# Performance work log

Measured on AMD Instinct MI355X. Metric: run time of the kernel, lower is better.

Reference implementation:

```python
import jax, jax.numpy as jnp
import numpy as np

B, N, K, D, H, PQ, PV = 2, 2048, 30, 128, 4, 8, 4
INV3C = float(np.sqrt(1.0 / (3 * D)))      # 1/sqrt(3*hidden_dim)
INV3 = float(np.sqrt(1.0 / 3.0))
PT_SCALE = float(np.sqrt(1.0 / (3 * (PQ * 9.0 / 2))))


def _gather(nodes, idx):
    # nodes [B,N,...], idx [B,N,K] -> [B,N,K,...]
    return jax.vmap(lambda n, i: n[i])(nodes, idx)


def _ln(x, w, b, eps=1e-5):
    mu = x.mean(-1, keepdims=True)
    var = x.var(-1, keepdims=True)
    return (x - mu) / jnp.sqrt(var + eps) * w + b


def _forward(h_V, h_E, E_idx, R, t, mask_attend, mask_V,
             Wq, bq, Wkv, bkv, Wqp, bqp, Wkvp, bkvp, Wb, bb_, head_weights,
             Wout, bout, ln0_w, ln0_b, ln1_w, ln1_b, Wm1, bm1, Wm2, bm2):
    q = (h_V @ Wq + bq).reshape(B, N, H, D)                     # [B,N,H,C]
    kv = (h_V @ Wkv + bkv).reshape(B, N, H, 2 * D)
    k_, v_ = kv[..., :D], kv[..., D:]

    def apply_rigid(pts):  # pts [B,N,P,3] -> R @ p + t
        return jnp.einsum('bnxy,bnpy->bnpx', R, pts) + t[:, :, None, :]

    # torch builds points by split-into-3-then-stack along last dim
    qp = h_V @ Wqp + bqp                                        # [B,N,H*PQ*3]
    q_pts = jnp.stack(jnp.split(qp, 3, axis=-1), axis=-1)       # [B,N,H*PQ,3]
    q_pts = apply_rigid(q_pts).reshape(B, N, H, PQ, 3)
    kvp = h_V @ Wkvp + bkvp
    kv_pts = jnp.stack(jnp.split(kvp, 3, axis=-1), axis=-1)
    kv_pts = apply_rigid(kv_pts).reshape(B, N, H, PQ + PV, 3)
    k_pts, v_pts = kv_pts[..., :PQ, :], kv_pts[..., PQ:, :]

    b_bias = h_E @ Wb + bb_                                     # [B,N,K,H]
    k_nb = _gather(k_, E_idx)                                   # [B,N,K,H,C]
    a = jnp.einsum('bnhc,bnkhc->bnkh', q, k_nb) * INV3C
    a = a + INV3 * b_bias

    kp_nb = _gather(k_pts, E_idx)                               # [B,N,K,H,PQ,3]
    diff = q_pts[:, :, None] - kp_nb
    pt_att = jnp.sum(diff * diff, axis=-1)                      # [B,N,K,H,PQ]
    hw = jax.nn.softplus(head_weights)                          # [H]
    pt_att = jnp.sum(PT_SCALE * hw[None, None, None, :, None] * pt_att, axis=-1) * -0.5

    att_mask = 100000.0 * (mask_attend - 1.0)                   # [B,N,K]
    a = a + pt_att + att_mask[..., None]
    a = jax.nn.softmax(a, axis=-2)                              # softmax over neighbors K

    v_nb = _gather(v_, E_idx)
    o = jnp.einsum('bnkh,bnkhc->bnhc', a, v_nb).reshape(B, N, H * D)
    vp_nb = _gather(v_pts, E_idx)                               # [B,N,K,H,PV,3]
    o_pt = jnp.einsum('bnkh,bnkhpx->bnhpx', a, vp_nb)
    # invert_apply: R^T (x - t)
    o_pt = jnp.einsum('bnyx,bnhpy->bnhpx', R, o_pt - t[:, :, None, None, :])
    o_pt_norm = jnp.sqrt(jnp.sum(o_pt ** 2, axis=-1) + 1e-8).reshape(B, N, H * PV)
    o_pt = o_pt.reshape(B, N, H * PV, 3)
    o_pair = jnp.einsum('bnkh,bnkc->bnhc', a, h_E).reshape(B, N, H * D)

    cat = jnp.concatenate([o, o_pt[..., 0], o_pt[..., 1], o_pt[..., 2], o_pt_norm, o_pair], axis=-1)
    s = cat @ Wout + bout

    hv = _ln(h_V + s, ln0_w, ln0_b)
    m = jax.nn.relu(hv @ Wm1 + bm1) @ Wm2 + bm2
    hv = _ln(hv + m, ln1_w, ln1_b)
    return hv * mask_V[..., None]


def setup_inputs() -> dict:
    key = jax.random.key(0)
    ks = jax.random.split(key, 16)

    def dense(k, fi, fo):
        kw, kb = jax.random.split(k)
        s = 1.0 / np.sqrt(fi)
        return (jax.random.uniform(kw, (fi, fo), jnp.float32, -s, s),
                jax.random.uniform(kb, (fo,), jnp.float32, -s, s))

    h_V = jax.random.normal(ks[0], (B, N, D), jnp.float32)
    h_E = jax.random.normal(ks[1], (B, N, K, D), jnp.float32)
    E_idx = jax.random.randint(ks[2], (B, N, K), 0, N)
    Rr = jax.random.normal(ks[3], (B, N, 3, 3), jnp.float32)
    R, _ = jnp.linalg.qr(Rr)  # proper orthonormal frames
    t = jax.random.normal(ks[4], (B, N, 3), jnp.float32)
    mask_attend = jnp.ones((B, N, K), jnp.float32)
    mask_V = jnp.ones((B, N), jnp.float32)

    Wq, bq = dense(ks[5], D, D * H)
    Wkv, bkv = dense(ks[6], D, 2 * D * H)
    Wqp, bqp = dense(ks[7], D, H * PQ * 3)
    Wkvp, bkvp = dense(ks[8], D, H * (PQ + PV) * 3)
    Wb, bb_ = dense(ks[9], D, H)
    head_weights = jnp.full((H,), 0.541324854612918, jnp.float32)
    out_dim = H * (D + D + 4 * PV)
    Wout, bout = dense(ks[10], out_dim, D)
    ln0_w = jnp.ones((D,), jnp.float32); ln0_b = jnp.zeros((D,), jnp.float32)
    ln1_w = jnp.ones((D,), jnp.float32); ln1_b = jnp.zeros((D,), jnp.float32)
    Wm1, bm1 = dense(ks[11], D, 4 * D)
    Wm2, bm2 = dense(ks[12], 4 * D, D)
    return dict(h_V=h_V, h_E=h_E, E_idx=E_idx, R=R, t=t,
                mask_attend=mask_attend, mask_V=mask_V,
                Wq=Wq, bq=bq, Wkv=Wkv, bkv=bkv, Wqp=Wqp, bqp=bqp,
                Wkvp=Wkvp, bkvp=bkvp, Wb=Wb, bb_=bb_, head_weights=head_weights,
                Wout=Wout, bout=bout, ln0_w=ln0_w, ln0_b=ln0_b,
                ln1_w=ln1_w, ln1_b=ln1_b, Wm1=Wm1, bm1=bm1, Wm2=Wm2, bm2=bm2)


def reference(h_V, h_E, E_idx, R, t, mask_attend, mask_V,
              Wq, bq, Wkv, bkv, Wqp, bqp, Wkvp, bkvp, Wb, bb_, head_weights,
              Wout, bout, ln0_w, ln0_b, ln1_w, ln1_b, Wm1, bm1, Wm2, bm2):
    return _forward(h_V, h_E, E_idx, R, t, mask_attend, mask_V,
                    Wq, bq, Wkv, bkv, Wqp, bqp, Wkvp, bkvp, Wb, bb_, head_weights,
                    Wout, bout, ln0_w, ln0_b, ln1_w, ln1_b, Wm1, bm1, Wm2, bm2)
```

## Files before the change

kernel.cpp:

```cpp
#include <hip/hip_runtime.h>
#include <math.h>

#define BB 2
#define NN 2048
#define KK 30
#define DD 128
#define HH 4
#define PQ_ 8
#define PV_ 4
#define TM 16

#define INV3C    0.05103103630798288f
#define INV3     0.5773502691896258f
#define PT_SCALE 0.09622504486493764f

typedef __attribute__((ext_vector_type(8))) short short8;
typedef __attribute__((ext_vector_type(4))) float f32x4;
typedef unsigned short ushort_t;

__device__ __forceinline__ ushort_t f2bf(float f) {
    unsigned u = __float_as_uint(f);
    unsigned r = u + 0x7FFFu + ((u >> 16) & 1u);
    return (ushort_t)(r >> 16);
}
__device__ __forceinline__ float bf2f(ushort_t u) {
    return __uint_as_float(((unsigned)u) << 16);
}
__device__ __forceinline__ float bflo(unsigned u) {
    return __uint_as_float(u << 16);
}
__device__ __forceinline__ float bfhi(unsigned u) {
    return __uint_as_float(u & 0xffff0000u);
}

__global__ __launch_bounds__(256) void prep_kernel(
    const float* __restrict__ Wout, const float* __restrict__ Wm1,
    const float* __restrict__ Wm2,
    const float* __restrict__ Wq, const float* __restrict__ Wkv,
    const float* __restrict__ Wqp, const float* __restrict__ Wkvp,
    ushort_t* __restrict__ WoutT, ushort_t* __restrict__ Wm1T,
    ushort_t* __restrict__ Wm2T, ushort_t* __restrict__ WprojT)
{
    const int stride = gridDim.x * blockDim.x;
    const int t0 = blockIdx.x * blockDim.x + threadIdx.x;
    for (int idx = t0; idx < 128 * 1088; idx += stride) {
        int n = idx / 1088, k = idx - n * 1088;
        WoutT[idx] = f2bf(Wout[(size_t)k * 128 + n]);
    }
    for (int idx = t0; idx < 512 * 128; idx += stride) {
        int n = idx >> 7, k = idx & 127;
        Wm1T[idx] = f2bf(Wm1[(size_t)k * 512 + n]);
    }
    for (int idx = t0; idx < 128 * 512; idx += stride) {
        int n = idx >> 9, k = idx & 511;
        Wm2T[idx] = f2bf(Wm2[(size_t)k * 128 + n]);
    }
    for (int idx = t0; idx < 1792 * 128; idx += stride) {
        int n = idx >> 7, k = idx & 127;
        float v;
        if (n < 512)       v = Wq[(size_t)k * 512 + n];
        else if (n < 1536) v = Wkv[(size_t)k * 1024 + (n - 512)];
        else if (n < 1632) v = Wqp[k * 96 + (n - 1536)];
        else if (n < 1776) v = Wkvp[k * 144 + (n - 1632)];
        else               v = 0.f;
        WprojT[idx] = f2bf(v);
    }
}

__global__ __launch_bounds__(512) void proj_kernel(
    const float* __restrict__ hV, const float* __restrict__ R, const float* __restrict__ tvec,
    const ushort_t* __restrict__ WT,
    const float* __restrict__ bq, const float* __restrict__ bkv,
    const float* __restrict__ bqp, const float* __restrict__ bkvp,
    ushort_t* __restrict__ qb, ushort_t* __restrict__ kb, ushort_t* __restrict__ vb,
    float* __restrict__ qpts, float* __restrict__ kpts, float* __restrict__ vpts)
{
    const int node0 = (blockIdx.x >> 1) * TM;
    const int half  = blockIdx.x & 1;
    const int tid = threadIdx.x;
    const int w = tid >> 6, l = tid & 63, lr = l & 15, lk = l >> 4;

    __shared__ ushort_t s_A[TM][128];
    __shared__ float s_qp[TM][96];
    __shared__ float s_kvp[TM][144];

    {
        int i = tid * 4; int r = i >> 7, c = i & 127;
        float4 x = *(const float4*)&hV[(size_t)(node0 + r) * DD + c];
        s_A[r][c + 0] = f2bf(x.x); s_A[r][c + 1] = f2bf(x.y);
        s_A[r][c + 2] = f2bf(x.z); s_A[r][c + 3] = f2bf(x.w);
    }
    __syncthreads();

    const ushort_t* Ab = &s_A[lr][lk * 8];
    for (int t = 0; t < 7; ++t) {
        const int tile = half * 56 + w * 7 + t;
        const int n = tile * 16 + lr;
        f32x4 acc = {0.f, 0.f, 0.f, 0.f};
        const ushort_t* Bb = WT + (size_t)n * 128 + lk * 8;
        #pragma unroll
        for (int ks = 0; ks < 4; ++ks) {
            short8 a = *(const short8*)(Ab + ks * 32);
            short8 bfr = *(const short8*)(Bb + ks * 32);
            acc = __builtin_amdgcn_mfma_f32_16x16x32_bf16(a, bfr, acc, 0, 0, 0);
        }
        if (n < 512) {
            float bias = bq[n];
            #pragma unroll
            for (int i = 0; i < 4; ++i)
                qb[(size_t)(node0 + lk * 4 + i) * 512 + n] = f2bf(acc[i] + bias);
        } else if (n < 1536) {
            int n2 = n - 512;
            float bias = bkv[n2];
            int hh = n2 >> 8, wcol = n2 & 255;
            ushort_t* base = (wcol < 128) ? kb : vb;
            int off = hh * DD + (wcol & 127);
            #pragma unroll
            for (int i = 0; i < 4; ++i)
                base[(size_t)(node0 + lk * 4 + i) * 512 + off] = f2bf(acc[i] + bias);
        } else if (n < 1632) {
            int c = n - 1536;
            float bias = bqp[c];
            #pragma unroll
            for (int i = 0; i < 4; ++i) s_qp[lk * 4 + i][c] = acc[i] + bias;
        } else if (n < 1776) {
            int c = n - 1632;
            float bias = bkvp[c];
            #pragma unroll
            for (int i = 0; i < 4; ++i) s_kvp[lk * 4 + i][c] = acc[i] + bias;
        }
    }
    __syncthreads();

    if (half == 1) {
        for (int idx = tid; idx < TM * 96; idx += 512) {
            int r = idx / 96, u = idx % 96;
            int j = u / 3, d = u % 3;
            int node = node0 + r;
            float acc = tvec[node * 3 + d];
            #pragma unroll
            for (int y = 0; y < 3; ++y)
                acc = fmaf(R[node * 9 + d * 3 + y], s_qp[r][y * 32 + j], acc);
            qpts[(size_t)node * 96 + j * 3 + d] = acc;
        }
        for (int idx = tid; idx < TM * 144; idx += 512) {
            int r = idx / 144, u = idx % 144;
            int jj = u / 3, d = u % 3;
            int node = node0 + r;
            float acc = tvec[node * 3 + d];
            #pragma unroll
            for (int y = 0; y < 3; ++y)
                acc = fmaf(R[node * 9 + d * 3 + y], s_kvp[r][y * 48 + jj], acc);
            int hh = jj / 12, pp = jj % 12;
            if (pp < PQ_) kpts[(size_t)node * 96 + (hh * PQ_ + pp) * 3 + d] = acc;
            else          vpts[(size_t)node * 48 + (hh * PV_ + (pp - PQ_)) * 3 + d] = acc;
        }
    }
}

__global__ __launch_bounds__(256, 6) void attn_kernel(
    const float* __restrict__ hE, const int* __restrict__ Eidx,
    const float* __restrict__ R, const float* __restrict__ tvec,
    const float* __restrict__ mask_att,
    const float* __restrict__ Wb, const float* __restrict__ bb,
    const float* __restrict__ head_w,
    const ushort_t* __restrict__ qb, const ushort_t* __restrict__ kb,
    const ushort_t* __restrict__ vb,
    const float* __restrict__ qpts, const float* __restrict__ kpts, const float* __restrict__ vpts,
    ushort_t* __restrict__ catb)
{
    const int node = blockIdx.x;
    const int b = node >> 11;
    const int tid = threadIdx.x;
    const int lane = tid & 63;
    const int wv = tid >> 6;

    __shared__ ushort_t s_hEb[KK * DD];
    __shared__ float s_cat[1088];
    __shared__ float s_qp[96];
    __shared__ float s_p[HH][32];
    __shared__ int   s_j[32];
    __shared__ float s_mask[32];
    __shared__ float s_opt[48];

    if (tid < 96) s_qp[tid] = qpts[(size_t)node * 96 + tid];
    if (tid < KK) {
        s_j[tid] = Eidx[(size_t)node * KK + tid];
        s_mask[tid] = 100000.0f * (mask_att[(size_t)node * KK + tid] - 1.0f);
    }
    __syncthreads();

    const int h = wv;
    const int l32 = lane & 31;
    const int g = lane >> 5;
    const float* hE_node = hE + (size_t)node * (KK * DD);

    const unsigned qu0 = *(const unsigned*)&qb[(size_t)node * 512 + h * DD + 2 * l32];
    const unsigned qu1 = *(const unsigned*)&qb[(size_t)node * 512 + h * DD + 64 + 2 * l32];
    const float q0 = bflo(qu0), q1 = bfhi(qu0), q2 = bflo(qu1), q3 = bfhi(qu1);
    const float wb0 = Wb[(l32 +  0) * HH + h];
    const float wb1 = Wb[(l32 + 32) * HH + h];
    const float wb2 = Wb[(l32 + 64) * HH + h];
    const float wb3 = Wb[(l32 + 96) * HH + h];
    const float cpt = -0.5f * PT_SCALE * log1pf(expf(head_w[h]));
    const float bbh = INV3 * bb[h];
    const float qpl = (l32 < 24) ? s_qp[h * 24 + l32] : 0.f;

    #pragma unroll
    for (int kx2 = 0; kx2 < KK / 2; ++kx2) {
        const int k = kx2 * 2 + g;
        size_t jb = (size_t)(b * NN + s_j[k]);
        const ushort_t* kr = kb + jb * 512 + h * DD;
        unsigned ku0 = *(const unsigned*)&kr[2 * l32];
        unsigned ku1 = *(const unsigned*)&kr[64 + 2 * l32];
        float s = q0 * bflo(ku0) + q1 * bfhi(ku0) + q2 * bflo(ku1) + q3 * bfhi(ku1);
        const float* her = hE_node + k * DD;
        float h0 = her[l32], h1 = her[l32 + 32], h2 = her[l32 + 64], h3 = her[l32 + 96];
        if (wv == 0) {
            s_hEb[k * DD + l32]      = f2bf(h0);
            s_hEb[k * DD + l32 + 32] = f2bf(h1);
            s_hEb[k * DD + l32 + 64] = f2bf(h2);
            s_hEb[k * DD + l32 + 96] = f2bf(h3);
        }
        float t = wb0 * h0 + wb1 * h1 + wb2 * h2 + wb3 * h3;
        float ptc = 0.f;
        if (l32 < 24) {
            float d = qpl - kpts[jb * 96 + h * 24 + l32];
            ptc = d * d;
        }
        float val = INV3C * s + INV3 * t + cpt * ptc;
        #pragma unroll
        for (int off = 16; off; off >>= 1) val += __shfl_down(val, off, 32);
        if (l32 == 0) s_p[h][k] = val + bbh + s_mask[k];
    }
    __syncthreads();

    {
        float v = (lane < KK) ? s_p[h][lane] : -INFINITY;
        float m = v;
        #pragma unroll
        for (int off = 16; off; off >>= 1) m = fmaxf(m, __shfl_down(m, off));
        m = __shfl(m, 0);
        float e = (lane < KK) ? expf(v - m) : 0.f;
        float s = e;
        #pragma unroll
        for (int off = 16; off; off >>= 1) s += __shfl_down(s, off);
        s = __shfl(s, 0);
        if (lane < KK) s_p[h][lane] = e / s;
    }
    __syncthreads();

    {
        const int oh = tid >> 6;
        const int oc0 = (tid & 63) * 2;
        const ushort_t* vrow = vb + oh * DD + oc0;
        float a0 = 0.f, a1 = 0.f, b0 = 0.f, b1 = 0.f;
        #pragma unroll
        for (int kx = 0; kx < KK; ++kx) {
            unsigned pv = *(const unsigned*)(vrow + (size_t)(b * NN + s_j[kx]) * 512);
            unsigned pe = *(const unsigned*)&s_hEb[kx * DD + oc0];
            float p = s_p[oh][kx];
            a0 = fmaf(p, bflo(pv), a0);
            a1 = fmaf(p, bfhi(pv), a1);
            b0 = fmaf(p, bflo(pe), b0);
            b1 = fmaf(p, bfhi(pe), b1);
        }
        s_cat[oh * DD + oc0]           = a0;
        s_cat[oh * DD + oc0 + 1]       = a1;
        s_cat[576 + oh * DD + oc0]     = b0;
        s_cat[576 + oh * DD + oc0 + 1] = b1;
    }
    if (tid < 48) {
        const int oh = (tid / 3) >> 2;
        float acc = 0.f;
        #pragma unroll
        for (int kx = 0; kx < KK; ++kx)
            acc = fmaf(s_p[oh][kx], vpts[(size_t)(b * NN + s_j[kx]) * 48 + tid], acc);
        s_opt[tid] = acc;
    }
    __syncthreads();
    if (tid < 16) {
        int jj = tid;
        float g0 = s_opt[jj * 3 + 0] - tvec[node * 3 + 0];
        float g1 = s_opt[jj * 3 + 1] - tvec[node * 3 + 1];
        float g2 = s_opt[jj * 3 + 2] - tvec[node * 3 + 2];
        float l0 = R[node * 9 + 0] * g0 + R[node * 9 + 3] * g1 + R[node * 9 + 6] * g2;
        float l1 = R[node * 9 + 1] * g0 + R[node * 9 + 4] * g1 + R[node * 9 + 7] * g2;
        float l2 = R[node * 9 + 2] * g0 + R[node * 9 + 5] * g1 + R[node * 9 + 8] * g2;
        s_cat[512 + 0 * 16 + jj] = l0;
        s_cat[512 + 1 * 16 + jj] = l1;
        s_cat[512 + 2 * 16 + jj] = l2;
        s_cat[560 + jj] = sqrtf(l0 * l0 + l1 * l1 + l2 * l2 + 1e-8f);
    }
    __syncthreads();

    for (int i = tid; i < 1088; i += 256)
        catb[(size_t)node * 1088 + i] = f2bf(s_cat[i]);
}

__global__ __launch_bounds__(512) void tail_kernel(
    const float* __restrict__ hV, const float* __restrict__ maskV,
    const ushort_t* __restrict__ catb,
    const ushort_t* __restrict__ WoutT, const float* __restrict__ bout,
    const float* __restrict__ ln0w, const float* __restrict__ ln0b,
    const float* __restrict__ ln1w, const float* __restrict__ ln1b,
    const ushort_t* __restrict__ Wm1T, const float* __restrict__ bm1,
    const ushort_t* __restrict__ Wm2T, const float* __restrict__ bm2,
    float* __restrict__ out)
{
    const int node0 = blockIdx.x * TM;
    const int tid = threadIdx.x;
    const int w  = tid >> 6;
    const int l  = tid & 63;
    const int lr = l & 15;
    const int lk = l >> 4;

    __shared__ float    s_x[TM][DD];
    __shared__ float    s_hv[TM][DD];
    __shared__ ushort_t s_hvb[TM][136];
    __shared__ ushort_t s_m1[TM][520];
    __shared__ float    s_rs[TM][16];
    __shared__ float    s_rq[TM][16];
    __shared__ float    s_stat[TM][2];

    {
        f32x4 acc = {0.f, 0.f, 0.f, 0.f};
        const ushort_t* Ab = catb + (size_t)(node0 + lr) * 1088 + lk * 8;
        const ushort_t* Bb = WoutT + (size_t)(w * 16 + lr) * 1088 + lk * 8;
        #pragma unroll 2
        for (int ks = 0; ks < 34; ++ks) {
            short8 a = *(const short8*)(Ab + ks * 32);
            short8 bfr = *(const short8*)(Bb + ks * 32);
            acc = __builtin_amdgcn_mfma_f32_16x16x32_bf16(a, bfr, acc, 0, 0, 0);
        }
        #pragma unroll
        for (int i = 0; i < 4; ++i)
            s_x[lk * 4 + i][w * 16 + lr] = acc[i];
    }
    __syncthreads();

    if (tid < 256) {
        int r = tid >> 4, sg = tid & 15;
        float ss = 0.f, sq = 0.f;
        #pragma unroll
        for (int j = 0; j < 8; ++j) {
            int cc = sg * 8 + j;
            float x = s_x[r][cc] + bout[cc] + hV[(size_t)(node0 + r) * DD + cc];
            s_x[r][cc] = x;
            ss += x; sq += x * x;
        }
        s_rs[r][sg] = ss; s_rq[r][sg] = sq;
    }
    __syncthreads();
    if (tid < TM) {
        float ss = 0.f, sq = 0.f;
        #pragma unroll
        for (int sg = 0; sg < 16; ++sg) { ss += s_rs[tid][sg]; sq += s_rq[tid][sg]; }
        float mu = ss / 128.f;
        s_stat[tid][0] = mu;
        s_stat[tid][1] = rsqrtf(sq / 128.f - mu * mu + 1e-5f);
    }
    __syncthreads();
    {
        int idx = tid * 4;
        int r = idx >> 7, cc = idx & 127;
        float mu = s_stat[r][0], rstd = s_stat[r][1];
        #pragma unroll
        for (int j = 0; j < 4; ++j) {
            float hvv = (s_x[r][cc + j] - mu) * rstd * ln0w[cc + j] + ln0b[cc + j];
            s_hv[r][cc + j] = hvv;
            s_hvb[r][cc + j] = f2bf(hvv);
        }
    }
    __syncthreads();

    {
        const ushort_t* Ab = &s_hvb[lr][lk * 8];
        #pragma unroll
        for (int t = 0; t < 4; ++t) {
            int n0 = w * 64 + t * 16;
            f32x4 acc = {0.f, 0.f, 0.f, 0.f};
            const ushort_t* Bb = Wm1T + (size_t)(n0 + lr) * 128 + lk * 8;
            #pragma unroll
            for (int ks = 0; ks < 4; ++ks) {
                short8 a = *(const short8*)(Ab + ks * 32);
                short8 bfr = *(const short8*)(Bb + ks * 32);
                acc = __builtin_amdgcn_mfma_f32_16x16x32_bf16(a, bfr, acc, 0, 0, 0);
            }
            int n = n0 + lr;
            float bm = bm1[n];
            #pragma unroll
            for (int i = 0; i < 4; ++i)
                s_m1[lk * 4 + i][n] = f2bf(fmaxf(acc[i] + bm, 0.f));
        }
    }
    __syncthreads();

    {
        f32x4 acc = {0.f, 0.f, 0.f, 0.f};
        const ushort_t* Ab = &s_m1[lr][lk * 8];
        const ushort_t* Bb = Wm2T + (size_t)(w * 16 + lr) * 512 + lk * 8;
        #pragma unroll 4
        for (int ks = 0; ks < 16; ++ks) {
            short8 a = *(const short8*)(Ab + ks * 32);
            short8 bfr = *(const short8*)(Bb + ks * 32);
            acc = __builtin_amdgcn_mfma_f32_16x16x32_bf16(a, bfr, acc, 0, 0, 0);
        }
        #pragma unroll
        for (int i = 0; i < 4; ++i)
            s_x[lk * 4 + i][w * 16 + lr] = acc[i];
    }
    __syncthreads();

    if (tid < 256) {
        int r = tid >> 4, sg = tid & 15;
        float ss = 0.f, sq = 0.f;
        #pragma unroll
        for (int j = 0; j < 8; ++j) {
            int cc = sg * 8 + j;
            float x = s_x[r][cc] + bm2[cc] + s_hv[r][cc];
            s_x[r][cc] = x;
            ss += x; sq += x * x;
        }
        s_rs[r][sg] = ss; s_rq[r][sg] = sq;
    }
    __syncthreads();
    if (tid < TM) {
        float ss = 0.f, sq = 0.f;
        #pragma unroll
        for (int sg = 0; sg < 16; ++sg) { ss += s_rs[tid][sg]; sq += s_rq[tid][sg]; }
        float mu = ss / 128.f;
        s_stat[tid][0] = mu;
        s_stat[tid][1] = rsqrtf(sq / 128.f - mu * mu + 1e-5f);
    }
    __syncthreads();
    {
        int idx = tid * 4;
        int r = idx >> 7, cc = idx & 127;
        float mu = s_stat[r][0], rstd = s_stat[r][1];
        float mk = maskV[node0 + r];
        float4 o;
        o.x = ((s_x[r][cc + 0] - mu) * rstd * ln1w[cc + 0] + ln1b[cc + 0]) * mk;
        o.y = ((s_x[r][cc + 1] - mu) * rstd * ln1w[cc + 1] + ln1b[cc + 1]) * mk;
        o.z = ((s_x[r][cc + 2] - mu) * rstd * ln1w[cc + 2] + ln1b[cc + 2]) * mk;
        o.w = ((s_x[r][cc + 3] - mu) * rstd * ln1w[cc + 3] + ln1b[cc + 3]) * mk;
        *(float4*)&out[(size_t)(node0 + r) * DD + cc] = o;
    }
}

extern "C" void kernel_launch(void* const* d_in, const int* in_sizes, int n_in,
                              void* d_out, int out_size, void* d_ws, size_t ws_size,
                              hipStream_t stream)
{
    const float* hV      = (const float*)d_in[0];
    const float* hE      = (const float*)d_in[1];
    const int*   Eidx    = (const int*)  d_in[2];
    const float* R       = (const float*)d_in[3];
    const float* tvec    = (const float*)d_in[4];
    const float* mask_at = (const float*)d_in[5];
    const float* maskV   = (const float*)d_in[6];
    const float* Wq      = (const float*)d_in[7];
    const float* bq      = (const float*)d_in[8];
    const float* Wkv     = (const float*)d_in[9];
    const float* bkv     = (const float*)d_in[10];
    const float* Wqp     = (const float*)d_in[11];
    const float* bqp     = (const float*)d_in[12];
    const float* Wkvp    = (const float*)d_in[13];
    const float* bkvp    = (const float*)d_in[14];
    const float* Wb      = (const float*)d_in[15];
    const float* bb      = (const float*)d_in[16];
    const float* hw      = (const float*)d_in[17];
    const float* Wout    = (const float*)d_in[18];
    const float* bout    = (const float*)d_in[19];
    const float* ln0w    = (const float*)d_in[20];
    const float* ln0b    = (const float*)d_in[21];
    const float* ln1w    = (const float*)d_in[22];
    const float* ln1b    = (const float*)d_in[23];
    const float* Wm1     = (const float*)d_in[24];
    const float* bm1     = (const float*)d_in[25];
    const float* Wm2     = (const float*)d_in[26];
    const float* bm2     = (const float*)d_in[27];

    const size_t nodes = (size_t)BB * NN;
    ushort_t* qb     = (ushort_t*)d_ws;
    ushort_t* kb     = qb + nodes * 512;
    ushort_t* vb     = kb + nodes * 512;
    ushort_t* catb   = vb + nodes * 512;
    ushort_t* WoutT  = catb + nodes * 1088;
    ushort_t* Wm1T   = WoutT + 128 * 1088;
    ushort_t* Wm2T   = Wm1T + 512 * 128;
    ushort_t* WprojT = Wm2T + 128 * 512;
    float* qpts = (float*)(WprojT + 1792 * 128);
    float* kpts = qpts + nodes * 96;
    float* vpts = kpts + nodes * 96;

    prep_kernel<<<256, 256, 0, stream>>>(Wout, Wm1, Wm2, Wq, Wkv, Wqp, Wkvp,
                                         WoutT, Wm1T, Wm2T, WprojT);

    proj_kernel<<<(int)(nodes / TM) * 2, 512, 0, stream>>>(
        hV, R, tvec, WprojT, bq, bkv, bqp, bkvp,
        qb, kb, vb, qpts, kpts, vpts);

    attn_kernel<<<(int)nodes, 256, 0, stream>>>(
        hE, Eidx, R, tvec, mask_at,
        Wb, bb, hw,
        qb, kb, vb, qpts, kpts, vpts, catb);

    tail_kernel<<<(int)(nodes / TM), 512, 0, stream>>>(
        hV, maskV, catb,
        WoutT, bout, ln0w, ln0b, ln1w, ln1b,
        Wm1T, bm1, Wm2T, bm2, (float*)d_out);
}
```

Baseline: 103.7 us.

## Vectorize attention gathers with 16-byte loads and pad value points to float4

Inside the attention kernel, each wave now handles four neighbors at once, with 16 lanes each issuing 16-byte (short8) loads of bf16 k/v rows. Before, every neighbor used 32-lane 4-byte loads. The h_E tile is converted to bf16 in shared memory up front, so the bias dot product reads it from LDS. Value points are stored padded to 4 floats per point so they can be gathered with float4 loads and folded into the same loop. The aim is fewer, wider global gathers and more memory parallelism, at the cost of extra cross-lane shuffle reductions and higher register use for the 8-wide accumulators.

```diff
diff --git a/kernel.cpp b/kernel.cpp
--- a/kernel.cpp
+++ b/kernel.cpp
@@ -25,12 +25,6 @@
 }
 __device__ __forceinline__ float bf2f(ushort_t u) {
     return __uint_as_float(((unsigned)u) << 16);
-}
-__device__ __forceinline__ float bflo(unsigned u) {
-    return __uint_as_float(u << 16);
-}
-__device__ __forceinline__ float bfhi(unsigned u) {
-    return __uint_as_float(u & 0xffff0000u);
 }
 
 __global__ __launch_bounds__(256) void prep_kernel(
@@ -153,7 +147,7 @@
                 acc = fmaf(R[node * 9 + d * 3 + y], s_kvp[r][y * 48 + jj], acc);
             int hh = jj / 12, pp = jj % 12;
             if (pp < PQ_) kpts[(size_t)node * 96 + (hh * PQ_ + pp) * 3 + d] = acc;
-            else          vpts[(size_t)node * 48 + (hh * PV_ + (pp - PQ_)) * 3 + d] = acc;
+            else          vpts[(size_t)node * 64 + (hh * PV_ + (pp - PQ_)) * 4 + d] = acc;
         }
     }
 }
@@ -174,6 +168,8 @@
     const int tid = threadIdx.x;
     const int lane = tid & 63;
     const int wv = tid >> 6;
+    const int l16 = lane & 15;
+    const int g4 = lane >> 4;
 
     __shared__ ushort_t s_hEb[KK * DD];
     __shared__ float s_cat[1088];
@@ -188,50 +184,56 @@
         s_j[tid] = Eidx[(size_t)node * KK + tid];
         s_mask[tid] = 100000.0f * (mask_att[(size_t)node * KK + tid] - 1.0f);
     }
+    const float* hE_node = hE + (size_t)node * (KK * DD);
+    #pragma unroll
+    for (int i = 0; i < 8; ++i) {
+        const int k = wv + i * 4;
+        if (k < KK) {
+            float2 hv2 = *(const float2*)&hE_node[k * DD + lane * 2];
+            unsigned pk = ((unsigned)f2bf(hv2.y) << 16) | (unsigned)f2bf(hv2.x);
+            *(unsigned*)&s_hEb[k * DD + lane * 2] = pk;
+        }
+    }
     __syncthreads();
 
     const int h = wv;
-    const int l32 = lane & 31;
-    const int g = lane >> 5;
-    const float* hE_node = hE + (size_t)node * (KK * DD);
-
-    const unsigned qu0 = *(const unsigned*)&qb[(size_t)node * 512 + h * DD + 2 * l32];
-    const unsigned qu1 = *(const unsigned*)&qb[(size_t)node * 512 + h * DD + 64 + 2 * l32];
-    const float q0 = bflo(qu0), q1 = bfhi(qu0), q2 = bflo(qu1), q3 = bfhi(qu1);
-    const float wb0 = Wb[(l32 +  0) * HH + h];
-    const float wb1 = Wb[(l32 + 32) * HH + h];
-    const float wb2 = Wb[(l32 + 64) * HH + h];
-    const float wb3 = Wb[(l32 + 96) * HH + h];
+    float qf[8], wbv[8];
+    {
+        short8 q8 = *(const short8*)&qb[(size_t)node * 512 + h * DD + l16 * 8];
+        #pragma unroll
+        for (int j = 0; j < 8; ++j) qf[j] = bf2f((ushort_t)q8[j]);
+    }
+    #pragma unroll
+    for (int j = 0; j < 8; ++j) wbv[j] = Wb[(l16 * 8 + j) * HH + h];
     const float cpt = -0.5f * PT_SCALE * log1pf(expf(head_w[h]));
     const float bbh = INV3 * bb[h];
-    const float qpl = (l32 < 24) ? s_qp[h * 24 + l32] : 0.f;
+    float2 qp2 = make_float2(0.f, 0.f);
+    if (l16 < 12) qp2 = *(const float2*)&s_qp[h * 24 + 2 * l16];
 
     #pragma unroll
-    for (int kx2 = 0; kx2 < KK / 2; ++kx2) {
-        const int k = kx2 * 2 + g;
-        size_t jb = (size_t)(b * NN + s_j[k]);
-        const ushort_t* kr = kb + jb * 512 + h * DD;
-        unsigned ku0 = *(const unsigned*)&kr[2 * l32];
-        unsigned ku1 = *(const unsigned*)&kr[64 + 2 * l32];
-        float s = q0 * bflo(ku0) + q1 * bfhi(ku0) + q2 * bflo(ku1) + q3 * bfhi(ku1);
-        const float* her = hE_node + k * DD;
-        float h0 = her[l32], h1 = her[l32 + 32], h2 = her[l32 + 64], h3 = her[l32 + 96];
-        if (wv == 0) {
-            s_hEb[k * DD + l32]      = f2bf(h0);
-            s_hEb[k * DD + l32 + 32] = f2bf(h1);
-            s_hEb[k * DD + l32 + 64] = f2bf(h2);
-            s_hEb[k * DD + l32 + 96] = f2bf(h3);
-        }
-        float t = wb0 * h0 + wb1 * h1 + wb2 * h2 + wb3 * h3;
-        float ptc = 0.f;
-        if (l32 < 24) {
-            float d = qpl - kpts[jb * 96 + h * 24 + l32];
-            ptc = d * d;
-        }
-        float val = INV3C * s + INV3 * t + cpt * ptc;
-        #pragma unroll
-        for (int off = 16; off; off >>= 1) val += __shfl_down(val, off, 32);
-        if (l32 == 0) s_p[h][k] = val + bbh + s_mask[k];
+    for (int i = 0; i < 8; ++i) {
+        const int k = i * 4 + g4;
+        if (k < KK) {
+            size_t jb = (size_t)(b * NN + s_j[k]);
+            short8 k8 = *(const short8*)&kb[jb * 512 + h * DD + l16 * 8];
+            short8 e8 = *(const short8*)&s_hEb[k * DD + l16 * 8];
+            float s = 0.f, t = 0.f;
+            #pragma unroll
+            for (int j = 0; j < 8; ++j) {
+                s = fmaf(qf[j], bf2f((ushort_t)k8[j]), s);
+                t = fmaf(wbv[j], bf2f((ushort_t)e8[j]), t);
+            }
+            float ptc = 0.f;
+            if (l16 < 12) {
+                float2 kp2 = *(const float2*)&kpts[jb * 96 + h * 24 + 2 * l16];
+                float d0 = qp2.x - kp2.x, d1 = qp2.y - kp2.y;
+                ptc = d0 * d0 + d1 * d1;
+            }
+            float val = INV3C * s + INV3 * t + cpt * ptc;
+            #pragma unroll
+            for (int off = 8; off; off >>= 1) val += __shfl_down(val, off, 16);
+            if (l16 == 0) s_p[h][k] = val + bbh + s_mask[k];
+        }
     }
     __syncthreads();
 
@@ -251,34 +253,55 @@
     __syncthreads();
 
     {
-        const int oh = tid >> 6;
-        const int oc0 = (tid & 63) * 2;
-        const ushort_t* vrow = vb + oh * DD + oc0;
-        float a0 = 0.f, a1 = 0.f, b0 = 0.f, b1 = 0.f;
-        #pragma unroll
-        for (int kx = 0; kx < KK; ++kx) {
-            unsigned pv = *(const unsigned*)(vrow + (size_t)(b * NN + s_j[kx]) * 512);
-            unsigned pe = *(const unsigned*)&s_hEb[kx * DD + oc0];
-            float p = s_p[oh][kx];
-            a0 = fmaf(p, bflo(pv), a0);
-            a1 = fmaf(p, bfhi(pv), a1);
-            b0 = fmaf(p, bflo(pe), b0);
-            b1 = fmaf(p, bfhi(pe), b1);
-        }
-        s_cat[oh * DD + oc0]           = a0;
-        s_cat[oh * DD + oc0 + 1]       = a1;
-        s_cat[576 + oh * DD + oc0]     = b0;
-        s_cat[576 + oh * DD + oc0 + 1] = b1;
-    }
-    if (tid < 48) {
-        const int oh = (tid / 3) >> 2;
-        float acc = 0.f;
-        #pragma unroll
-        for (int kx = 0; kx < KK; ++kx)
-            acc = fmaf(s_p[oh][kx], vpts[(size_t)(b * NN + s_j[kx]) * 48 + tid], acc);
-        s_opt[tid] = acc;
-    }
-    __syncthreads();
+        float a[8], bp[8];
+        #pragma unroll
+        for (int j = 0; j < 8; ++j) { a[j] = 0.f; bp[j] = 0.f; }
+        float p0 = 0.f, p1 = 0.f, p2 = 0.f;
+        const int pj = h * PV_ + l16;
+        #pragma unroll
+        for (int i = 0; i < 8; ++i) {
+            const int kx = i * 4 + g4;
+            if (kx < KK) {
+                size_t jb = (size_t)(b * NN + s_j[kx]);
+                short8 v8 = *(const short8*)&vb[jb * 512 + h * DD + l16 * 8];
+                short8 e8 = *(const short8*)&s_hEb[kx * DD + l16 * 8];
+                float p = s_p[h][kx];
+                #pragma unroll
+                for (int j = 0; j < 8; ++j) {
+                    a[j]  = fmaf(p, bf2f((ushort_t)v8[j]), a[j]);
+                    bp[j] = fmaf(p, bf2f((ushort_t)e8[j]), bp[j]);
+                }
+                if (l16 < 4) {
+                    float4 vp4 = *(const float4*)&vpts[jb * 64 + pj * 4];
+                    p0 = fmaf(p, vp4.x, p0);
+                    p1 = fmaf(p, vp4.y, p1);
+                    p2 = fmaf(p, vp4.z, p2);
+                }
+            }
+        }
+        #pragma unroll
+        for (int j = 0; j < 8; ++j) {
+            a[j]  += __shfl_down(a[j], 32);  a[j]  += __shfl_down(a[j], 16);
+            bp[j] += __shfl_down(bp[j], 32); bp[j] += __shfl_down(bp[j], 16);
+        }
+        p0 += __shfl_down(p0, 32); p0 += __shfl_down(p0, 16);
+        p1 += __shfl_down(p1, 32); p1 += __shfl_down(p1, 16);
+        p2 += __shfl_down(p2, 32); p2 += __shfl_down(p2, 16);
+        if (g4 == 0) {
+            #pragma unroll
+            for (int j = 0; j < 8; ++j) {
+                s_cat[h * DD + l16 * 8 + j]       = a[j];
+                s_cat[576 + h * DD + l16 * 8 + j] = bp[j];
+            }
+            if (l16 < 4) {
+                s_opt[pj * 3 + 0] = p0;
+                s_opt[pj * 3 + 1] = p1;
+                s_opt[pj * 3 + 2] = p2;
+            }
+        }
+    }
+    __syncthreads();
+
     if (tid < 16) {
         int jj = tid;
         float g0 = s_opt[jj * 3 + 0] - tvec[node * 3 + 0];
```

New measurement: 164.3 us. +58.5%, slower.
